# Kernel optimization log

Measured on AMD Instinct MI355X. Metric: run time of the kernel, lower is better.

## Reference

```python
import jax, jax.numpy as jnp
import numpy as np

D = 1024
H = 16
DH = D // H


def setup_inputs() -> dict:
    key = jax.random.key(0)
    ks = jax.random.split(key, 5)
    x = jax.random.normal(ks[0], (2, 2048, D), dtype=jnp.float32)
    s = 1.0 / np.sqrt(D)
    W_qkv = jax.random.normal(ks[1], (D, 3 * D), dtype=jnp.float32) * s
    b_qkv = jnp.zeros((3 * D,), dtype=jnp.float32)
    W_out = jax.random.normal(ks[2], (D, D), dtype=jnp.float32) * s
    b_out = jnp.zeros((D,), dtype=jnp.float32)
    return {"x": x, "W_qkv": W_qkv, "b_qkv": b_qkv, "W_out": W_out, "b_out": b_out}


def reference(x, W_qkv, b_qkv, W_out, b_out):
    B, N, _ = x.shape
    qkv = x @ W_qkv + b_qkv                       # [B,N,3D]
    qkv = qkv.reshape(B, N, 3, H, DH)
    q = jnp.transpose(qkv[:, :, 0], (0, 2, 1, 3))  # [B,H,N,DH]
    k = jnp.transpose(qkv[:, :, 1], (0, 2, 1, 3))
    v = jnp.transpose(qkv[:, :, 2], (0, 2, 1, 3))
    scores = jnp.einsum('bhnd,bhmd->bhnm', q, k) / jnp.sqrt(jnp.float32(DH))
    attn = jax.nn.softmax(scores, axis=-1)
    out = jnp.einsum('bhnm,bhmd->bhnd', attn, v)   # [B,H,N,DH]
    out = jnp.transpose(out, (0, 2, 1, 3)).reshape(B, N, D)
    return out @ W_out + b_out
```

## Files before the change

kernel.cpp:

```cpp
#include <hip/hip_runtime.h>

typedef unsigned short u16;
typedef unsigned int u32;
typedef __attribute__((ext_vector_type(8))) short bf16x8;
typedef __attribute__((ext_vector_type(4))) float f32x4;

static __device__ __forceinline__ void mfma16(f32x4& c, bf16x8 a, bf16x8 b) {
  asm("v_mfma_f32_16x16x32_bf16 %0, %1, %2, %0" : "+v"(c) : "v"(a), "v"(b));
}
static __device__ __forceinline__ float exp2_fast(float x) {
  float r; asm("v_exp_f32 %0, %1" : "=v"(r) : "v"(x)); return r;
}
static __device__ __forceinline__ u32 cvt_pk_bf16(float lo, float hi) {
  u32 r; asm("v_cvt_pk_bf16_f32 %0, %1, %2" : "=v"(r) : "v"(lo), "v"(hi)); return r;
}

static __device__ __forceinline__ float bfly_sum(float x) {
  x += __shfl_xor(x, 16);
  x += __shfl_xor(x, 32);
  return x;
}

static __device__ __forceinline__ u16 f2bf(float f) {
  union { float f; u32 u; } v; v.f = f;
  u32 r = v.u + 0x7fffu + ((v.u >> 16) & 1u);
  return (u16)(r >> 16);
}

typedef __attribute__((address_space(1))) void as1_v;
typedef __attribute__((address_space(3))) void as3_v;
static __device__ __forceinline__ void gload16(const u16* g, u16* l) {
  __builtin_amdgcn_global_load_lds((as1_v*)g, (as3_v*)l, 16, 0, 0);
}

__global__ __launch_bounds__(256) void cvt_bf16(const float* __restrict__ in,
                                                u16* __restrict__ out, int n4) {
  int i = blockIdx.x * 256 + threadIdx.x;
  if (i < n4) {
    float4 f = ((const float4*)in)[i];
    ushort4 u;
    u.x = f2bf(f.x); u.y = f2bf(f.y); u.z = f2bf(f.z); u.w = f2bf(f.w);
    ((ushort4*)out)[i] = u;
  }
}

__global__ __launch_bounds__(256) void transpose_cvt(const float* __restrict__ W,
                                                     u16* __restrict__ Wt,
                                                     int K, int Nc) {
  __shared__ float tile[32][33];
  int nb = blockIdx.x * 32, kb = blockIdx.y * 32;
  int tx = threadIdx.x, ty = threadIdx.y;
  for (int i = ty; i < 32; i += 8)
    tile[i][tx] = W[(size_t)(kb + i) * Nc + nb + tx];
  __syncthreads();
  for (int i = ty; i < 32; i += 8)
    Wt[(size_t)(nb + i) * K + kb + tx] = f2bf(tile[tx][i]);
}

__global__ __launch_bounds__(256) void vtrans(const u16* __restrict__ qkv,
                                              u16* __restrict__ vt) {
  __shared__ u16 t[64][72];
  const int tid = threadIdx.x;
  const int bh = blockIdx.y, nt = blockIdx.x;
  const int b = bh >> 4, h = bh & 15;
  const int n0 = nt * 64;
  const int r = tid >> 3, c = tid & 7;
  const u16* src = qkv + (size_t)(b * 2048 + n0 + r) * 3072 + 2048 + h * 64;
  *(int4*)&t[r][(c ^ ((r >> 3) & 7)) * 8] = *(const int4*)(src + c * 8);
  const u16* src2 = src + (size_t)32 * 3072;
  *(int4*)&t[r + 32][(c ^ (((r + 32) >> 3) & 7)) * 8] = *(const int4*)(src2 + c * 8);
  __syncthreads();
  const int d = tid >> 3, j0 = (tid & 7) * 8;
  union { int4 v; u16 u[8]; } o0, o1;
#pragma unroll
  for (int j = 0; j < 8; ++j) {
    const int row = j0 + j;
    const int sw = (row >> 3) & 7;
    o0.u[j] = t[row][((d >> 3) ^ sw) * 8 + (d & 7)];
    o1.u[j] = t[row][(((d + 32) >> 3) ^ sw) * 8 + ((d + 32) & 7)];
  }
  u16* dst = vt + (size_t)bh * 131072 + (size_t)d * 2048 + n0 + j0;
  *(int4*)dst = o0.v;
  *(int4*)(dst + (size_t)32 * 2048) = o1.v;
}

template <int OUT_F32>
__global__ __launch_bounds__(256) void gemm_bt(const u16* __restrict__ A,
                                               const u16* __restrict__ Bt,
                                               const float* __restrict__ bias,
                                               void* __restrict__ C,
                                               int M, int N, int K,
                                               float qscale, int qcols) {
  __shared__ u16 lA[2][4096];
  __shared__ u16 lB[2][4096];
  const int tid = threadIdx.x;
  const int lane = tid & 63, wid = tid >> 6;
  const int nbx = N >> 7;
  const int per = ((M >> 7) * nbx) >> 3;
  const int g = (blockIdx.x & 7) * per + (blockIdx.x >> 3);
  const int bx = g % nbx, by = g / nbx;
  const int m0 = by << 7, n0 = bx << 7;
  const int wr = wid >> 1, wc = wid & 1;

  const int srow = tid >> 2;
  const int scol = (tid & 3) << 3;
  const u16* gA0 = A + (size_t)(m0 + srow) * K + scol;
  const u16* gA1 = A + (size_t)(m0 + 64 + srow) * K + scol;
  const u16* gB0 = Bt + (size_t)(n0 + srow) * K + scol;
  const u16* gB1 = Bt + (size_t)(n0 + 64 + srow) * K + scol;

  const int rdA = (wr * 64 + (lane & 15)) * 32 + ((lane >> 4) * 8);
  const int rdB = (wc * 64 + (lane & 15)) * 32 + ((lane >> 4) * 8);

  f32x4 acc[4][4] = {};

  gload16(gA0, &lA[0][tid * 8]);
  gload16(gA1, &lA[0][2048 + tid * 8]);
  gload16(gB0, &lB[0][tid * 8]);
  gload16(gB1, &lB[0][2048 + tid * 8]);
  __syncthreads();

  const int nk = K >> 5;
  for (int t = 0; t < nk; ++t) {
    const int cur = t & 1, nxt = cur ^ 1;
    if (t + 1 < nk) {
      const int k0 = (t + 1) << 5;
      gload16(gA0 + k0, &lA[nxt][tid * 8]);
      gload16(gA1 + k0, &lA[nxt][2048 + tid * 8]);
      gload16(gB0 + k0, &lB[nxt][tid * 8]);
      gload16(gB1 + k0, &lB[nxt][2048 + tid * 8]);
    }
    bf16x8 aF[4], bF[4];
#pragma unroll
    for (int m = 0; m < 4; ++m) aF[m] = *(const bf16x8*)(&lA[cur][rdA + m * 512]);
#pragma unroll
    for (int n = 0; n < 4; ++n) bF[n] = *(const bf16x8*)(&lB[cur][rdB + n * 512]);
#pragma unroll
    for (int m = 0; m < 4; ++m)
#pragma unroll
      for (int n = 0; n < 4; ++n) mfma16(acc[m][n], aF[m], bF[n]);
    __syncthreads();
  }

#pragma unroll
  for (int n = 0; n < 4; ++n) {
    const int col = n0 + wc * 64 + n * 16 + (lane & 15);
    const float bv = bias[col];
    const float sc = (col < qcols) ? qscale : 1.0f;
#pragma unroll
    for (int m = 0; m < 4; ++m) {
      const int rbase = m0 + wr * 64 + m * 16 + ((lane >> 4) * 4);
#pragma unroll
      for (int r = 0; r < 4; ++r) {
        const float v = (acc[m][n][r] + bv) * sc;
        const size_t idx = (size_t)(rbase + r) * N + col;
        if (OUT_F32) ((float*)C)[idx] = v;
        else         ((u16*)C)[idx] = f2bf(v);
      }
    }
  }
}

__global__ __launch_bounds__(256) void attn_kernel(const u16* __restrict__ qkv,
                                                   const u16* __restrict__ vt,
                                                   u16* __restrict__ attn_out) {
  __shared__ u16 lK[2][4096];
  __shared__ u16 lV[2][4096];

  const int tid = threadIdx.x, lane = tid & 63, w = tid >> 6;
  const int l15 = lane & 15, g = lane >> 4;
  const int bid = blockIdx.x;
  const int tt = bid >> 3;
  const int qt = tt & 31;
  const int bh = ((tt >> 5) << 3) | (bid & 7);
  const int b = bh >> 4, h = bh & 15;

  const size_t rowQ = (size_t)(b * 2048 + qt * 64 + w * 16 + l15);
  const u16* qptr = qkv + rowQ * 3072 + h * 64 + g * 8;
  const bf16x8 qf0 = *(const bf16x8*)(qptr);
  const bf16x8 qf1 = *(const bf16x8*)(qptr + 32);

  const int r0 = tid >> 3, r1 = 32 + (tid >> 3);
  const int c0 = (tid & 7) ^ ((r0 ^ (r0 >> 3)) & 7);
  const int c1 = (tid & 7) ^ ((r1 ^ (r1 >> 3)) & 7);
  const u16* gk0 = qkv + (size_t)(b * 2048 + r0) * 3072 + 1024 + h * 64 + c0 * 8;
  const u16* gk1 = qkv + (size_t)(b * 2048 + r1) * 3072 + 1024 + h * 64 + c1 * 8;
  const u16* vtb = vt + (size_t)bh * 131072;
  const u16* gv0 = vtb + (size_t)r0 * 2048 + c0 * 8;
  const u16* gv1 = vtb + (size_t)r1 * 2048 + c1 * 8;

  int koff[4][2];
#pragma unroll
  for (int f = 0; f < 4; ++f) {
    const int R = 32 * (f >> 1) + 8 * (l15 >> 2) + 4 * ((l15 >> 1) & 1) +
                  2 * (f & 1) + (l15 & 1);
    const int sw = (R ^ (R >> 3)) & 7;
#pragma unroll
    for (int hf = 0; hf < 2; ++hf)
      koff[f][hf] = R * 64 + ((((hf << 2) | g) ^ sw) << 3);
  }
  int voff[4][2];
#pragma unroll
  for (int d = 0; d < 4; ++d) {
    const int R = d * 16 + l15;
    const int sw = (R ^ (R >> 3)) & 7;
#pragma unroll
    for (int kk = 0; kk < 2; ++kk)
      voff[d][kk] = R * 64 + ((((kk << 2) | g) ^ sw) << 3);
  }

  float lp = 0.f;
  f32x4 oacc[4] = {};

  gload16(gk0, &lK[0][tid * 8]);
  gload16(gk1, &lK[0][2048 + tid * 8]);
  gload16(gv0, &lV[0][tid * 8]);
  gload16(gv1, &lV[0][2048 + tid * 8]);
  __syncthreads();

  for (int it = 0; it < 32; ++it) {
    const int cur = it & 1, nxt = cur ^ 1;
    const u16* Kc = lK[cur];
    const u16* Vc = lV[cur];
    if (it + 1 < 32) {
      const size_t ko = (size_t)(it + 1) * 64 * 3072;
      const int vo = (it + 1) * 64;
      gload16(gk0 + ko, &lK[nxt][tid * 8]);
      gload16(gk1 + ko, &lK[nxt][2048 + tid * 8]);
      gload16(gv0 + vo, &lV[nxt][tid * 8]);
      gload16(gv1 + vo, &lV[nxt][2048 + tid * 8]);
    }

    f32x4 s[4] = {};
#pragma unroll
    for (int f = 0; f < 4; ++f) {
      mfma16(s[f], *(const bf16x8*)(Kc + koff[f][0]), qf0);
      mfma16(s[f], *(const bf16x8*)(Kc + koff[f][1]), qf1);
    }

#pragma unroll
    for (int f = 0; f < 4; ++f)
#pragma unroll
      for (int r = 0; r < 4; ++r) s[f][r] = exp2_fast(s[f][r]);
    lp += (((s[0][0] + s[0][1]) + (s[0][2] + s[0][3])) +
           ((s[1][0] + s[1][1]) + (s[1][2] + s[1][3]))) +
          (((s[2][0] + s[2][1]) + (s[2][2] + s[2][3])) +
           ((s[3][0] + s[3][1]) + (s[3][2] + s[3][3])));

    union { bf16x8 v; u32 u[4]; } p0, p1;
    p0.u[0] = cvt_pk_bf16(s[0][0], s[0][1]);
    p0.u[1] = cvt_pk_bf16(s[1][0], s[1][1]);
    p0.u[2] = cvt_pk_bf16(s[0][2], s[0][3]);
    p0.u[3] = cvt_pk_bf16(s[1][2], s[1][3]);
    p1.u[0] = cvt_pk_bf16(s[2][0], s[2][1]);
    p1.u[1] = cvt_pk_bf16(s[3][0], s[3][1]);
    p1.u[2] = cvt_pk_bf16(s[2][2], s[2][3]);
    p1.u[3] = cvt_pk_bf16(s[3][2], s[3][3]);

#pragma unroll
    for (int d = 0; d < 4; ++d) {
      mfma16(oacc[d], *(const bf16x8*)(Vc + voff[d][0]), p0.v);
      mfma16(oacc[d], *(const bf16x8*)(Vc + voff[d][1]), p1.v);
    }

    __syncthreads();
  }

  const float l_ = bfly_sum(lp);
  const float inv = 1.f / l_;
#pragma unroll
  for (int d = 0; d < 4; ++d)
#pragma unroll
    for (int r = 0; r < 4; ++r)
      attn_out[rowQ * 1024 + h * 64 + d * 16 + g * 4 + r] = f2bf(oacc[d][r] * inv);
}

extern "C" void kernel_launch(void* const* d_in, const int* in_sizes, int n_in,
                              void* d_out, int out_size, void* d_ws, size_t ws_size,
                              hipStream_t stream) {
  const float* x    = (const float*)d_in[0];
  const float* Wqkv = (const float*)d_in[1];
  const float* bqkv = (const float*)d_in[2];
  const float* Wout = (const float*)d_in[3];
  const float* bout = (const float*)d_in[4];
  float* out = (float*)d_out;

  char* ws = (char*)d_ws;
  u16* xb    = (u16*)(ws);
  u16* vt    = (u16*)(ws);
  u16* WqkvT = (u16*)(ws + 8388608);
  u16* WoutT = (u16*)(ws + 14680064);
  u16* qkvb  = (u16*)(ws + 16777216);
  u16* attnb = (u16*)(ws + 41943040);

  cvt_bf16<<<4096, 256, 0, stream>>>(x, xb, 4194304 / 4);
  transpose_cvt<<<dim3(96, 32), dim3(32, 8), 0, stream>>>(Wqkv, WqkvT, 1024, 3072);
  transpose_cvt<<<dim3(32, 32), dim3(32, 8), 0, stream>>>(Wout, WoutT, 1024, 1024);

  gemm_bt<0><<<dim3(24 * 32), 256, 0, stream>>>(xb, WqkvT, bqkv, qkvb,
                                                4096, 3072, 1024, 0.18033688f, 1024);
  vtrans<<<dim3(32, 32), 256, 0, stream>>>(qkvb, vt);
  attn_kernel<<<dim3(32 * 32), 256, 0, stream>>>(qkvb, vt, attnb);
  gemm_bt<1><<<dim3(8 * 32), 256, 0, stream>>>(attnb, WoutT, bout, out,
                                               4096, 1024, 1024, 1.0f, 0);
}
```

Measured before the change: 132.1 us.

## Split attention waves over query pairs and key halves with LDS reduction

Each block's four waves are regrouped into two query groups of 32 rows and two halves of the 64-key tile. Each wave reuses its K and V fragments across two 16-row query subtiles, which halves LDS fragment reads per MFMA. The two key-half partial outputs and row sums are combined through shared memory at the end. The MFMA inline asm is also replaced with the compiler builtin so the compiler can schedule it. The cost is more accumulator registers, an extra barrier and reduction pass, and only half the waves doing the final store.

Result: slower. 135.0 us (+2.2%).

```diff
diff --git a/kernel.cpp b/kernel.cpp
--- a/kernel.cpp
+++ b/kernel.cpp
@@ -3,10 +3,14 @@
 typedef unsigned short u16;
 typedef unsigned int u32;
 typedef __attribute__((ext_vector_type(8))) short bf16x8;
+typedef __attribute__((ext_vector_type(8))) __bf16 bf16v8;
 typedef __attribute__((ext_vector_type(4))) float f32x4;
 
 static __device__ __forceinline__ void mfma16(f32x4& c, bf16x8 a, bf16x8 b) {
   asm("v_mfma_f32_16x16x32_bf16 %0, %1, %2, %0" : "+v"(c) : "v"(a), "v"(b));
+}
+static __device__ __forceinline__ void mfma16b(f32x4& c, bf16v8 a, bf16v8 b) {
+  c = __builtin_amdgcn_mfma_f32_16x16x32_bf16(a, b, c, 0, 0, 0);
 }
 static __device__ __forceinline__ float exp2_fast(float x) {
   float r; asm("v_exp_f32 %0, %1" : "=v"(r) : "v"(x)); return r;
@@ -169,16 +173,20 @@
 
   const int tid = threadIdx.x, lane = tid & 63, w = tid >> 6;
   const int l15 = lane & 15, g = lane >> 4;
+  const int wq = w & 1, wk = w >> 1;
   const int bid = blockIdx.x;
   const int tt = bid >> 3;
   const int qt = tt & 31;
   const int bh = ((tt >> 5) << 3) | (bid & 7);
   const int b = bh >> 4, h = bh & 15;
 
-  const size_t rowQ = (size_t)(b * 2048 + qt * 64 + w * 16 + l15);
-  const u16* qptr = qkv + rowQ * 3072 + h * 64 + g * 8;
-  const bf16x8 qf0 = *(const bf16x8*)(qptr);
-  const bf16x8 qf1 = *(const bf16x8*)(qptr + 32);
+  const int qbase = b * 2048 + qt * 64 + wq * 32;
+  const u16* qp0 = qkv + (size_t)(qbase + l15) * 3072 + h * 64 + g * 8;
+  const u16* qp1 = qkv + (size_t)(qbase + 16 + l15) * 3072 + h * 64 + g * 8;
+  const bf16v8 qf00 = *(const bf16v8*)(qp0);
+  const bf16v8 qf01 = *(const bf16v8*)(qp0 + 32);
+  const bf16v8 qf10 = *(const bf16v8*)(qp1);
+  const bf16v8 qf11 = *(const bf16v8*)(qp1 + 32);
 
   const int r0 = tid >> 3, r1 = 32 + (tid >> 3);
   const int c0 = (tid & 7) ^ ((r0 ^ (r0 >> 3)) & 7);
@@ -189,28 +197,25 @@
   const u16* gv0 = vtb + (size_t)r0 * 2048 + c0 * 8;
   const u16* gv1 = vtb + (size_t)r1 * 2048 + c1 * 8;
 
-  int koff[4][2];
-#pragma unroll
-  for (int f = 0; f < 4; ++f) {
-    const int R = 32 * (f >> 1) + 8 * (l15 >> 2) + 4 * ((l15 >> 1) & 1) +
-                  2 * (f & 1) + (l15 & 1);
+  int koff[2][2];
+#pragma unroll
+  for (int f = 0; f < 2; ++f) {
+    const int R = wk * 32 + 8 * (l15 >> 2) + 4 * ((l15 >> 1) & 1) + 2 * f + (l15 & 1);
     const int sw = (R ^ (R >> 3)) & 7;
 #pragma unroll
     for (int hf = 0; hf < 2; ++hf)
       koff[f][hf] = R * 64 + ((((hf << 2) | g) ^ sw) << 3);
   }
-  int voff[4][2];
+  int voff[4];
 #pragma unroll
   for (int d = 0; d < 4; ++d) {
     const int R = d * 16 + l15;
     const int sw = (R ^ (R >> 3)) & 7;
-#pragma unroll
-    for (int kk = 0; kk < 2; ++kk)
-      voff[d][kk] = R * 64 + ((((kk << 2) | g) ^ sw) << 3);
-  }
-
-  float lp = 0.f;
-  f32x4 oacc[4] = {};
+    voff[d] = R * 64 + ((((wk << 2) | g) ^ sw) << 3);
+  }
+
+  float lp0 = 0.f, lp1 = 0.f;
+  f32x4 oacc[4][2] = {};
 
   gload16(gk0, &lK[0][tid * 8]);
   gload16(gk1, &lK[0][2048 + tid * 8]);
@@ -231,48 +236,83 @@
       gload16(gv1 + vo, &lV[nxt][2048 + tid * 8]);
     }
 
-    f32x4 s[4] = {};
-#pragma unroll
-    for (int f = 0; f < 4; ++f) {
-      mfma16(s[f], *(const bf16x8*)(Kc + koff[f][0]), qf0);
-      mfma16(s[f], *(const bf16x8*)(Kc + koff[f][1]), qf1);
-    }
-
-#pragma unroll
-    for (int f = 0; f < 4; ++f)
-#pragma unroll
-      for (int r = 0; r < 4; ++r) s[f][r] = exp2_fast(s[f][r]);
-    lp += (((s[0][0] + s[0][1]) + (s[0][2] + s[0][3])) +
-           ((s[1][0] + s[1][1]) + (s[1][2] + s[1][3]))) +
-          (((s[2][0] + s[2][1]) + (s[2][2] + s[2][3])) +
-           ((s[3][0] + s[3][1]) + (s[3][2] + s[3][3])));
-
-    union { bf16x8 v; u32 u[4]; } p0, p1;
-    p0.u[0] = cvt_pk_bf16(s[0][0], s[0][1]);
-    p0.u[1] = cvt_pk_bf16(s[1][0], s[1][1]);
-    p0.u[2] = cvt_pk_bf16(s[0][2], s[0][3]);
-    p0.u[3] = cvt_pk_bf16(s[1][2], s[1][3]);
-    p1.u[0] = cvt_pk_bf16(s[2][0], s[2][1]);
-    p1.u[1] = cvt_pk_bf16(s[3][0], s[3][1]);
-    p1.u[2] = cvt_pk_bf16(s[2][2], s[2][3]);
-    p1.u[3] = cvt_pk_bf16(s[3][2], s[3][3]);
+    const bf16v8 k00 = *(const bf16v8*)(Kc + koff[0][0]);
+    const bf16v8 k01 = *(const bf16v8*)(Kc + koff[0][1]);
+    const bf16v8 k10 = *(const bf16v8*)(Kc + koff[1][0]);
+    const bf16v8 k11 = *(const bf16v8*)(Kc + koff[1][1]);
+    f32x4 s00 = {}, s01 = {}, s10 = {}, s11 = {};
+    mfma16b(s00, k00, qf00); mfma16b(s00, k01, qf01);
+    mfma16b(s01, k10, qf00); mfma16b(s01, k11, qf01);
+    mfma16b(s10, k00, qf10); mfma16b(s10, k01, qf11);
+    mfma16b(s11, k10, qf10); mfma16b(s11, k11, qf11);
+
+#pragma unroll
+    for (int r = 0; r < 4; ++r) {
+      s00[r] = exp2_fast(s00[r]); s01[r] = exp2_fast(s01[r]);
+      s10[r] = exp2_fast(s10[r]); s11[r] = exp2_fast(s11[r]);
+    }
+    lp0 += ((s00[0] + s00[1]) + (s00[2] + s00[3])) +
+           ((s01[0] + s01[1]) + (s01[2] + s01[3]));
+    lp1 += ((s10[0] + s10[1]) + (s10[2] + s10[3])) +
+           ((s11[0] + s11[1]) + (s11[2] + s11[3]));
+
+    union { bf16v8 v; u32 u[4]; } p0, p1;
+    p0.u[0] = cvt_pk_bf16(s00[0], s00[1]);
+    p0.u[1] = cvt_pk_bf16(s01[0], s01[1]);
+    p0.u[2] = cvt_pk_bf16(s00[2], s00[3]);
+    p0.u[3] = cvt_pk_bf16(s01[2], s01[3]);
+    p1.u[0] = cvt_pk_bf16(s10[0], s10[1]);
+    p1.u[1] = cvt_pk_bf16(s11[0], s11[1]);
+    p1.u[2] = cvt_pk_bf16(s10[2], s10[3]);
+    p1.u[3] = cvt_pk_bf16(s11[2], s11[3]);
 
 #pragma unroll
     for (int d = 0; d < 4; ++d) {
-      mfma16(oacc[d], *(const bf16x8*)(Vc + voff[d][0]), p0.v);
-      mfma16(oacc[d], *(const bf16x8*)(Vc + voff[d][1]), p1.v);
+      const bf16v8 vf = *(const bf16v8*)(Vc + voff[d]);
+      mfma16b(oacc[d][0], vf, p0.v);
+      mfma16b(oacc[d][1], vf, p1.v);
     }
 
     __syncthreads();
   }
 
-  const float l_ = bfly_sum(lp);
-  const float inv = 1.f / l_;
-#pragma unroll
-  for (int d = 0; d < 4; ++d)
-#pragma unroll
-    for (int r = 0; r < 4; ++r)
-      attn_out[rowQ * 1024 + h * 64 + d * 16 + g * 4 + r] = f2bf(oacc[d][r] * inv);
+  float* cb = (float*)lK;
+  float* cl = (float*)lV;
+  const int ci = (wq << 6) | lane;
+  if (wk == 1) {
+#pragma unroll
+    for (int qg = 0; qg < 2; ++qg)
+#pragma unroll
+      for (int d = 0; d < 4; ++d)
+#pragma unroll
+        for (int i = 0; i < 4; ++i)
+          cb[ci * 32 + qg * 16 + d * 4 + i] = oacc[d][qg][i];
+    cl[ci * 2 + 0] = lp0;
+    cl[ci * 2 + 1] = lp1;
+  }
+  __syncthreads();
+  if (wk == 0) {
+#pragma unroll
+    for (int qg = 0; qg < 2; ++qg)
+#pragma unroll
+      for (int d = 0; d < 4; ++d)
+#pragma unroll
+        for (int i = 0; i < 4; ++i)
+          oacc[d][qg][i] += cb[ci * 32 + qg * 16 + d * 4 + i];
+    lp0 += cl[ci * 2 + 0];
+    lp1 += cl[ci * 2 + 1];
+    const float inv0 = 1.f / bfly_sum(lp0);
+    const float inv1 = 1.f / bfly_sum(lp1);
+    u16* op0 = attn_out + (size_t)(qbase + l15) * 1024 + h * 64 + g * 4;
+    u16* op1 = attn_out + (size_t)(qbase + 16 + l15) * 1024 + h * 64 + g * 4;
+#pragma unroll
+    for (int d = 0; d < 4; ++d)
+#pragma unroll
+      for (int r = 0; r < 4; ++r) {
+        op0[d * 16 + r] = f2bf(oacc[d][0][r] * inv0);
+        op1[d * 16 + r] = f2bf(oacc[d][1][r] * inv1);
+      }
+  }
 }
 
 extern "C" void kernel_launch(void* const* d_in, const int* in_sizes, int n_in,
```
